# Kernel tuning notes

Measured on AMD Instinct MI355X. Metric: run time of the kernel, lower is better.

The kernel has to match this reference:

```python
import jax, jax.numpy as jnp
import numpy as np

NEG_SLOPE = 0.01  # nn.LeakyReLU default
N_NODES = 38332
POI_LEN = 38333
CAT_LEN = 400
POI_DIM = 300
CAT_DIM = 100
GCN_CH = 64
GCN_LAYERS = 5
N_EDGES = N_NODES * 32


def leaky(x):
    return jnp.where(x >= 0, x, NEG_SLOPE * x)


def gcn_conv(x, src, dst, W, b):
    """PyG GCNConv: add self loops + symmetric normalization.
    out = D^-1/2 (A+I) D^-1/2 X W + b, deg computed with self loops."""
    n = x.shape[0]
    h = x @ W  # [N, out]
    deg = jax.ops.segment_sum(jnp.ones_like(dst, dtype=h.dtype), dst, num_segments=n) + 1.0
    dinv = jax.lax.rsqrt(deg)  # deg >= 1 always (self loop)
    norm = dinv[src] * dinv[dst]  # [E]
    agg = jax.ops.segment_sum(h[src] * norm[:, None], dst, num_segments=n)
    agg = agg + h * (1.0 / deg)[:, None]  # self-loop term: norm_ii = 1/deg_i
    return agg + b


def setup_inputs() -> dict:
    key = jax.random.key(0)
    ks = jax.random.split(key, 16)
    poi_ids = jax.random.randint(ks[0], (N_NODES, 1), 0, POI_LEN).astype(jnp.float32)
    cat_ids = jax.random.randint(ks[1], (N_NODES, 1), 0, CAT_LEN).astype(jnp.float32)
    feats = jax.random.normal(ks[2], (N_NODES, 3), dtype=jnp.float32)
    x = jnp.concatenate([poi_ids, cat_ids, feats], axis=1)  # [N,5]
    edge_index = jax.random.randint(ks[3], (2, N_EDGES), 0, N_NODES, dtype=jnp.int32)

    def glorot(k, shape):
        lim = float(np.sqrt(6.0 / (shape[0] + shape[1])))
        return jax.random.uniform(k, shape, jnp.float32, -lim, lim)

    d_in = POI_DIM + CAT_DIM + 3  # 403
    params = {
        "poi_emb": jax.random.normal(ks[4], (POI_LEN, POI_DIM), jnp.float32),
        "cat_emb": jax.random.normal(ks[5], (CAT_LEN, CAT_DIM), jnp.float32),
        "W_in": glorot(ks[6], (d_in, GCN_CH)),
        "b_in": jnp.zeros((GCN_CH,), jnp.float32),
        "gcn_Ws": jnp.stack([glorot(jax.random.fold_in(ks[7], i), (GCN_CH, GCN_CH)) for i in range(GCN_LAYERS)]),
        "gcn_bs": jnp.zeros((GCN_LAYERS, GCN_CH), jnp.float32),
        "W_out": glorot(ks[8], (GCN_CH, 1)),
        "b_out": jnp.zeros((1,), jnp.float32),
        "fc1_W": glorot(ks[9], (N_NODES, 128)),
        "fc1_b": jnp.zeros((128,), jnp.float32),
        "fc2_W": glorot(ks[10], (128, POI_LEN)),
        "fc2_b": jnpos if False else jnp.zeros((POI_LEN,), jnp.float32),
    }
    return {"x": x, "edge_index": edge_index, **params}


def reference(x, edge_index, poi_emb, cat_emb, W_in, b_in, gcn_Ws, gcn_bs, W_out, b_out, fc1_W, fc1_b, fc2_W, fc2_b):
    src, dst = edge_index[0], edge_index[1]
    poi_f = poi_emb[x[:, 0].astype(jnp.int32)]  # [N,300]
    cat_f = cat_emb[x[:, 1].astype(jnp.int32)]  # [N,100]
    feat = jnp.concatenate([poi_f, cat_f, x[:, 2:5]], axis=1)  # [N,403]
    feat = leaky(gcn_conv(feat, src, dst, W_in, b_in))
    for i in range(GCN_LAYERS):
        t = gcn_conv(feat, src, dst, gcn_Ws[i], gcn_bs[i])
        feat = leaky(t) + t  # GcnUnit: relu(temp) + temp
    feat = leaky(gcn_conv(feat, src, dst, W_out, b_out)).reshape(-1)  # [N]
    h = jax.nn.relu(feat @ fc1_W + fc1_b)
    out = jax.nn.relu(h @ fc2_W + fc2_b)  # [poi_len]
    return out
```

## Files before the change

### kernel.cpp

```cpp
#include <hip/hip_runtime.h>
#include <hip/hip_bf16.h>

#define N_NODES 38332
#define POI_LEN 38333
#define CAT_LEN 400
#define POI_DIM 300
#define CAT_DIM 100
#define N_EDGES (N_NODES * 32)
#define NEG_SLOPE 0.01f
#define B1 ((N_NODES + 127) / 128)
#define SPLIT_CHUNK 4096
#define NSPLIT ((N_EDGES + SPLIT_CHUNK - 1) / SPLIT_CHUNK)
#define PLACE_CAP 8192
#define BCAP 8192

typedef __attribute__((ext_vector_type(8))) short short8;
typedef __attribute__((ext_vector_type(4))) float f32x4;

__device__ __forceinline__ unsigned short f2bf(float f) {
  unsigned u = __float_as_uint(f);
  u += 0x7fff + ((u >> 16) & 1);
  return (unsigned short)(u >> 16);
}
__device__ __forceinline__ float bflo(unsigned u) {
  return __uint_as_float(u << 16);
}
__device__ __forceinline__ float bfhi(unsigned u) {
  return __uint_as_float(u & 0xffff0000u);
}


#define WFIN_ELEMS (13 * 2048)
#define WFGCN_ELEMS (5 * 4096)

__global__ __launch_bounds__(256) void k_prep(const float* __restrict__ W_in,
                                              const float* __restrict__ gcn_Ws,
                                              unsigned short* __restrict__ wf_in,
                                              unsigned short* __restrict__ wf_gcn,
                                              int* __restrict__ bcnt,
                                              float* __restrict__ h128) {
  int idx = blockIdx.x * 256 + threadIdx.x;
  if (idx < B1) bcnt[idx] = 0;
  if (idx < 128) h128[idx] = 0.f;
  if (idx < WFIN_ELEMS) {
    int j = idx & 7, n = (idx >> 3) & 63, q = (idx >> 9) & 3, ks = idx >> 11;
    int k = ks * 32 + q * 8 + j;
    wf_in[idx] = f2bf((k < 400) ? W_in[k * 64 + n] : 0.f);
  } else if (idx < WFIN_ELEMS + WFGCN_ELEMS) {
    int t = idx - WFIN_ELEMS;
    int l = t >> 12, i = t & 4095;
    int j = i & 7, n = (i >> 3) & 63, q = (i >> 9) & 3, ks = i >> 11;
    int k = ks * 32 + q * 8 + j;
    wf_gcn[t] = f2bf(gcn_Ws[(size_t)l * 4096 + k * 64 + n]);
  }
}


__global__ __launch_bounds__(256) void k_split(const int* __restrict__ src,
                                               const int* __restrict__ dst,
                                               int* __restrict__ bcnt,
                                               int* __restrict__ staging) {
  __shared__ int hist[B1];
  __shared__ int lbase[B1];
  __shared__ int lcur[B1];
  int tid = threadIdx.x;
  int base = blockIdx.x * SPLIT_CHUNK;
  int n = N_EDGES - base;
  if (n > SPLIT_CHUNK) n = SPLIT_CHUNK;
  for (int b = tid; b < B1; b += 256) {
    hist[b] = 0;
    lcur[b] = 0;
  }
  __syncthreads();
  for (int i = tid; i < n; i += 256) atomicAdd(&hist[dst[base + i] >> 7], 1);
  __syncthreads();
  for (int b = tid; b < B1; b += 256) {
    int c = hist[b];
    lbase[b] = c ? atomicAdd(&bcnt[b], c) : 0;
  }
  __syncthreads();
  for (int i = tid; i < n; i += 256) {
    int d = dst[base + i];
    int s = src[base + i];
    int b = d >> 7;
    int off = atomicAdd(&lcur[b], 1);
    staging[(size_t)b * BCAP + lbase[b] + off] = (s << 7) | (d & 127);
  }
}

__global__ __launch_bounds__(256) void k_place(const int* __restrict__ staging,
                                               const int* __restrict__ bcnt,
                                               int* __restrict__ csr_src,
                                               int2* __restrict__ rs,
                                               float* __restrict__ dinv) {
  __shared__ int lc[128];
  __shared__ int ls[256];
  __shared__ int cur[128];
  __shared__ int buf[PLACE_CAP];
  int b = blockIdx.x;
  int tid = threadIdx.x;
  int d0 = b * 128;
  int nd = N_NODES - d0;
  if (nd > 128) nd = 128;
  int cnt_b = bcnt[b];
  const int* st = staging + (size_t)b * BCAP;
  if (tid < 128) lc[tid] = 0;
  __syncthreads();
  for (int i = tid; i < cnt_b; i += 256) atomicAdd(&lc[st[i] & 127], 1);
  __syncthreads();
  int v = (tid < 128) ? lc[tid] : 0;
  ls[tid] = v;
  __syncthreads();
  for (int off = 1; off < 128; off <<= 1) {
    int t = (tid >= off) ? ls[tid - off] : 0;
    __syncthreads();
    ls[tid] += t;
    __syncthreads();
  }
  if (tid < 128) {
    int excl = ls[tid] - v;
    cur[tid] = excl;
    if (tid < nd) {
      rs[d0 + tid] = make_int2(b * BCAP + excl, v);
      dinv[d0 + tid] = 1.0f / sqrtf((float)(v + 1));
    }
  }
  __syncthreads();
  for (int i = tid; i < cnt_b; i += 256) {
    int p = st[i];
    int pos = atomicAdd(&cur[p & 127], 1);
    buf[pos] = p >> 7;
  }
  __syncthreads();
  int base = b * BCAP;
  for (int i = tid; i < cnt_b; i += 256) csr_src[base + i] = buf[i];
}


__global__ __launch_bounds__(256) void k_front(
    const float* __restrict__ x, const float* __restrict__ poi_emb,
    const float* __restrict__ cat_emb, const float* __restrict__ W_in,
    const unsigned short* __restrict__ wf_in, const float* __restrict__ dinv,
    unsigned short* __restrict__ hs) {
  constexpr int KP = 416, RS = 424, NK4 = 104;
  __shared__ unsigned short sA[16 * RS];
  __shared__ float sC[16 * 68];
  __shared__ int sPid[16], sCid[16];
  __shared__ float sX[16][3];
  int tid = threadIdx.x;
  int row0 = blockIdx.x * 16;
  if (tid < 16) {
    int row = row0 + tid;
    if (row < N_NODES) {
      sPid[tid] = (int)x[row * 5 + 0];
      sCid[tid] = (int)x[row * 5 + 1];
      sX[tid][0] = x[row * 5 + 2];
      sX[tid][1] = x[row * 5 + 3];
      sX[tid][2] = x[row * 5 + 4];
    } else {
      sPid[tid] = 0; sCid[tid] = 0;
      sX[tid][0] = sX[tid][1] = sX[tid][2] = 0.f;
    }
  }
  __syncthreads();
  for (int idx = tid; idx < 16 * NK4; idx += 256) {
    int r = idx / NK4;
    int k = (idx - r * NK4) * 4;
    ushort4 o = {0, 0, 0, 0};
    if (k < 400 && row0 + r < N_NODES) {
      float4 f;
      if (k < 300) f = *(const float4*)(poi_emb + (size_t)sPid[r] * 300 + k);
      else         f = *(const float4*)(cat_emb + (size_t)sCid[r] * 100 + (k - 300));
      o.x = f2bf(f.x); o.y = f2bf(f.y); o.z = f2bf(f.z); o.w = f2bf(f.w);
    }
    *(ushort4*)&sA[r * RS + k] = o;
  }
  __syncthreads();
  int lane = tid & 63, wv = tid >> 6;
  int c = lane & 15, q = lane >> 4, n0 = wv * 16;
  f32x4 acc = {0.f, 0.f, 0.f, 0.f};
  const unsigned short* arow = &sA[c * RS];
#pragma unroll
  for (int ks = 0; ks < KP / 32; ks++) {
    short8 af = *(const short8*)(arow + ks * 32 + q * 8);
    short8 bf = *(const short8*)(wf_in + ((size_t)((ks * 4 + q) * 64 + n0 + c)) * 8);
    acc = __builtin_amdgcn_mfma_f32_16x16x32_bf16(af, bf, acc, 0, 0, 0);
  }
#pragma unroll
  for (int r = 0; r < 4; r++) sC[(q * 4 + r) * 68 + n0 + c] = acc[r];
  __syncthreads();
  for (int idx = tid; idx < 16 * 64; idx += 256) {
    int r = idx >> 6, col = idx & 63;
    int row = row0 + r;
    if (row < N_NODES) {
      float v = sC[r * 68 + col] + sX[r][0] * W_in[400 * 64 + col] +
                sX[r][1] * W_in[401 * 64 + col] + sX[r][2] * W_in[402 * 64 + col];
      hs[(size_t)row * 64 + col] = f2bf(v * dinv[row]);
    }
  }
}


__global__ __launch_bounds__(256) void k_projg(const unsigned short* __restrict__ A,
                                               const unsigned short* __restrict__ Wf,
                                               unsigned short* __restrict__ hs,
                                               const float* __restrict__ dinv) {
  constexpr int RS = 72;
  __shared__ unsigned short sA[16 * RS];
  __shared__ float sC[16 * 68];
  int tid = threadIdx.x;
  int row0 = blockIdx.x * 16;
  {
    int r = tid >> 4, k4 = (tid & 15) * 4;
    int row = row0 + r;
    ushort4 o = {0, 0, 0, 0};
    if (row < N_NODES) o = *(const ushort4*)(A + (size_t)row * 64 + k4);
    *(ushort4*)&sA[r * RS + k4] = o;
  }
  __syncthreads();
  int lane = tid & 63, wv = tid >> 6;
  int c = lane & 15, q = lane >> 4, n0 = wv * 16;
  f32x4 acc = {0.f, 0.f, 0.f, 0.f};
  const unsigned short* arow = &sA[c * RS];
#pragma unroll
  for (int ks = 0; ks < 2; ks++) {
    short8 af = *(const short8*)(arow + ks * 32 + q * 8);
    short8 bf = *(const short8*)(Wf + ((size_t)((ks * 4 + q) * 64 + n0 + c)) * 8);
    acc = __builtin_amdgcn_mfma_f32_16x16x32_bf16(af, bf, acc, 0, 0, 0);
  }
#pragma unroll
  for (int r = 0; r < 4; r++) sC[(q * 4 + r) * 68 + n0 + c] = acc[r];
  __syncthreads();
  for (int idx = tid; idx < 16 * 64; idx += 256) {
    int r = idx >> 6, col = idx & 63;
    int row = row0 + r;
    if (row < N_NODES) hs[(size_t)row * 64 + col] = f2bf(sC[r * 68 + col] * dinv[row]);
  }
}


template <int MODE>
__global__ __launch_bounds__(256) void k_agg(const unsigned short* __restrict__ hs,
                                             const int2* __restrict__ rs,
                                             const int* __restrict__ csr_src,
                                             const float* __restrict__ dinv,
                                             const float* __restrict__ bias,
                                             unsigned short* __restrict__ feat,
                                             const float* __restrict__ W_out,
                                             float* __restrict__ hs1) {
  int tid = threadIdx.x;
  int lane = tid & 63;
  int wv = tid >> 6;
  int node = blockIdx.x * 4 + wv;
  int eslot = lane >> 3;
  int ch8 = lane & 7;
  int2 rr = rs[node];
  int r0 = rr.x, r1 = rr.x + rr.y;
  float4 a0 = {0.f, 0.f, 0.f, 0.f}, a1 = a0;
#define ACC8(v)                                                              \
  do {                                                                       \
    a0.x += bflo((v).x); a0.y += bfhi((v).x);                                \
    a0.z += bflo((v).y); a0.w += bfhi((v).y);                                \
    a1.x += bflo((v).z); a1.y += bfhi((v).z);                                \
    a1.z += bflo((v).w); a1.w += bfhi((v).w);                                \
  } while (0)
  int e = r0 + eslot;
  for (; e + 24 < r1; e += 32) {
    int s0 = csr_src[e];
    int s1 = csr_src[e + 8];
    int s2 = csr_src[e + 16];
    int s3 = csr_src[e + 24];
    uint4 v0 = *(const uint4*)(hs + (size_t)s0 * 64 + ch8 * 8);
    uint4 v1 = *(const uint4*)(hs + (size_t)s1 * 64 + ch8 * 8);
    uint4 v2 = *(const uint4*)(hs + (size_t)s2 * 64 + ch8 * 8);
    uint4 v3 = *(const uint4*)(hs + (size_t)s3 * 64 + ch8 * 8);
    ACC8(v0); ACC8(v1); ACC8(v2); ACC8(v3);
  }
  if (e + 8 < r1) {
    int s0 = csr_src[e];
    int s1 = csr_src[e + 8];
    uint4 v0 = *(const uint4*)(hs + (size_t)s0 * 64 + ch8 * 8);
    uint4 v1 = *(const uint4*)(hs + (size_t)s1 * 64 + ch8 * 8);
    ACC8(v0); ACC8(v1);
    e += 16;
  }
  if (e < r1) {
    int s = csr_src[e];
    uint4 v = *(const uint4*)(hs + (size_t)s * 64 + ch8 * 8);
    ACC8(v);
  }
#undef ACC8
#pragma unroll
  for (int off = 8; off <= 32; off <<= 1) {
    a0.x += __shfl_xor(a0.x, off, 64);
    a0.y += __shfl_xor(a0.y, off, 64);
    a0.z += __shfl_xor(a0.z, off, 64);
    a0.w += __shfl_xor(a0.w, off, 64);
    a1.x += __shfl_xor(a1.x, off, 64);
    a1.y += __shfl_xor(a1.y, off, 64);
    a1.z += __shfl_xor(a1.z, off, 64);
    a1.w += __shfl_xor(a1.w, off, 64);
  }
  if (lane < 8) {
    uint4 sv = *(const uint4*)(hs + (size_t)node * 64 + ch8 * 8);
    float4 bb0 = *(const float4*)(bias + ch8 * 8);
    float4 bb1 = *(const float4*)(bias + ch8 * 8 + 4);
    float dn = dinv[node];
    float4 t0, t1;
    t0.x = dn * (a0.x + bflo(sv.x)) + bb0.x;
    t0.y = dn * (a0.y + bfhi(sv.x)) + bb0.y;
    t0.z = dn * (a0.z + bflo(sv.y)) + bb0.z;
    t0.w = dn * (a0.w + bfhi(sv.y)) + bb0.w;
    t1.x = dn * (a1.x + bflo(sv.z)) + bb1.x;
    t1.y = dn * (a1.y + bfhi(sv.z)) + bb1.y;
    t1.z = dn * (a1.z + bflo(sv.w)) + bb1.z;
    t1.w = dn * (a1.w + bfhi(sv.w)) + bb1.w;
    float4 l0, l1, o0, o1;
    l0.x = (t0.x >= 0.f) ? t0.x : NEG_SLOPE * t0.x;
    l0.y = (t0.y >= 0.f) ? t0.y : NEG_SLOPE * t0.y;
    l0.z = (t0.z >= 0.f) ? t0.z : NEG_SLOPE * t0.z;
    l0.w = (t0.w >= 0.f) ? t0.w : NEG_SLOPE * t0.w;
    l1.x = (t1.x >= 0.f) ? t1.x : NEG_SLOPE * t1.x;
    l1.y = (t1.y >= 0.f) ? t1.y : NEG_SLOPE * t1.y;
    l1.z = (t1.z >= 0.f) ? t1.z : NEG_SLOPE * t1.z;
    l1.w = (t1.w >= 0.f) ? t1.w : NEG_SLOPE * t1.w;
    if (MODE == 0) {
      o0 = l0; o1 = l1;
    } else {
      o0.x = l0.x + t0.x; o0.y = l0.y + t0.y; o0.z = l0.z + t0.z; o0.w = l0.w + t0.w;
      o1.x = l1.x + t1.x; o1.y = l1.y + t1.y; o1.z = l1.z + t1.z; o1.w = l1.w + t1.w;
    }
    if (MODE == 2) {
      float4 w0 = *(const float4*)(W_out + ch8 * 8);
      float4 w1 = *(const float4*)(W_out + ch8 * 8 + 4);
      float p = o0.x * w0.x + o0.y * w0.y + o0.z * w0.z + o0.w * w0.w +
                o1.x * w1.x + o1.y * w1.y + o1.z * w1.z + o1.w * w1.w;
      p += __shfl_xor(p, 1, 64);
      p += __shfl_xor(p, 2, 64);
      p += __shfl_xor(p, 4, 64);
      if (lane == 0) hs1[node] = p * dn;
    } else {
      uint4 pk;
      pk.x = (unsigned)f2bf(o0.x) | ((unsigned)f2bf(o0.y) << 16);
      pk.y = (unsigned)f2bf(o0.z) | ((unsigned)f2bf(o0.w) << 16);
      pk.z = (unsigned)f2bf(o1.x) | ((unsigned)f2bf(o1.y) << 16);
      pk.w = (unsigned)f2bf(o1.z) | ((unsigned)f2bf(o1.w) << 16);
      *(uint4*)(feat + (size_t)node * 64 + ch8 * 8) = pk;
    }
  }
}


__global__ __launch_bounds__(256) void k_out_agg(const float* __restrict__ hs1,
                                                 const int2* __restrict__ rs,
                                                 const int* __restrict__ csr_src,
                                                 const float* __restrict__ dinv,
                                                 const float* __restrict__ b_out,
                                                 float* __restrict__ g) {
  int lane = threadIdx.x & 63;
  int w = threadIdx.x >> 6;
  int node = blockIdx.x * 4 + w;
  int2 rr = rs[node];
  int r0 = rr.x, r1 = rr.x + rr.y;
  float acc = 0.f;
  for (int e = r0 + lane; e < r1; e += 64) acc += hs1[csr_src[e]];
#pragma unroll
  for (int off = 32; off; off >>= 1) acc += __shfl_xor(acc, off, 64);
  if (lane == 0) {
    float t = dinv[node] * (acc + hs1[node]) + b_out[0];
    g[node] = (t >= 0.f) ? t : NEG_SLOPE * t;
  }
}


__global__ __launch_bounds__(128) void k_fc1(const float* __restrict__ g,
                                             const float* __restrict__ fc1_W,
                                             float* __restrict__ h128) {
  int j = threadIdx.x;
  int base = blockIdx.x * 32;
  int end = base + 32;
  if (end > N_NODES) end = N_NODES;
  float acc = 0.f;
  int i = base;
  for (; i + 4 <= end; i += 4) {
    acc += g[i + 0] * fc1_W[(size_t)(i + 0) * 128 + j];
    acc += g[i + 1] * fc1_W[(size_t)(i + 1) * 128 + j];
    acc += g[i + 2] * fc1_W[(size_t)(i + 2) * 128 + j];
    acc += g[i + 3] * fc1_W[(size_t)(i + 3) * 128 + j];
  }
  for (; i < end; i++) acc += g[i] * fc1_W[(size_t)i * 128 + j];
  atomicAdd(&h128[j], acc);
}

__global__ __launch_bounds__(256) void k_fc2(const float* __restrict__ h128raw,
                                             const float* __restrict__ fc1_b,
                                             const float* __restrict__ fc2_W,
                                             const float* __restrict__ fc2_b,
                                             float* __restrict__ out) {
  __shared__ float sh[128];
  int tid = threadIdx.x;
  if (tid < 128) {
    float v = h128raw[tid] + fc1_b[tid];
    sh[tid] = (v > 0.f) ? v : 0.f;
  }
  __syncthreads();
  int p = blockIdx.x * 256 + tid;
  if (p < POI_LEN) {
    float acc = fc2_b[p];
#pragma unroll 8
    for (int j = 0; j < 128; j++) acc += sh[j] * fc2_W[(size_t)j * POI_LEN + p];
    out[p] = (acc > 0.f) ? acc : 0.f;
  }
}


extern "C" void kernel_launch(void* const* d_in, const int* in_sizes, int n_in,
                              void* d_out, int out_size, void* d_ws, size_t ws_size,
                              hipStream_t stream) {
  const float* x       = (const float*)d_in[0];
  const int*   ei      = (const int*)d_in[1];
  const float* poi_emb = (const float*)d_in[2];
  const float* cat_emb = (const float*)d_in[3];
  const float* W_in    = (const float*)d_in[4];
  const float* b_in    = (const float*)d_in[5];
  const float* gcn_Ws  = (const float*)d_in[6];
  const float* gcn_bs  = (const float*)d_in[7];
  const float* W_out   = (const float*)d_in[8];
  const float* b_out   = (const float*)d_in[9];
  const float* fc1_W   = (const float*)d_in[10];
  const float* fc1_b   = (const float*)d_in[11];
  const float* fc2_W   = (const float*)d_in[12];
  const float* fc2_b   = (const float*)d_in[13];
  const int* src = ei;
  const int* dst = ei + N_EDGES;

  char* p = (char*)d_ws;
  auto take = [&](size_t bytes) {
    char* r = p;
    p += (bytes + 255) & ~(size_t)255;
    return r;
  };
  int2*  rs        = (int2*)take((size_t)N_NODES * 8);
  float* dinv      = (float*)take((size_t)N_NODES * 4);
  int*   bcnt      = (int*)take((size_t)B1 * 4);
  int*   csr_src   = (int*)take((size_t)B1 * BCAP * 4);
  unsigned short* feat = (unsigned short*)take((size_t)N_NODES * 64 * 2);
  unsigned short* hs   = (unsigned short*)take((size_t)N_NODES * 64 * 2);
  float* hs1       = (float*)take((size_t)N_NODES * 4);
  float* g         = (float*)take((size_t)N_NODES * 4);
  float* h128      = (float*)take(128 * 4);
  unsigned short* wf_in  = (unsigned short*)take((size_t)WFIN_ELEMS * 2);
  unsigned short* wf_gcn = (unsigned short*)take((size_t)WFGCN_ELEMS * 2);
  int* staging = (int*)feat;
  float* out = (float*)d_out;

  const int nb4 = N_NODES / 4;
  const int nb16 = (N_NODES + 15) / 16;

  k_prep<<<(WFIN_ELEMS + WFGCN_ELEMS + 255) / 256, 256, 0, stream>>>(
      W_in, gcn_Ws, wf_in, wf_gcn, bcnt, h128);
  k_split<<<NSPLIT, 256, 0, stream>>>(src, dst, bcnt, staging);
  k_place<<<B1, 256, 0, stream>>>(staging, bcnt, csr_src, rs, dinv);

  k_front<<<nb16, 256, 0, stream>>>(x, poi_emb, cat_emb, W_in, wf_in, dinv, hs);

  k_agg<0><<<nb4, 256, 0, stream>>>(hs, rs, csr_src, dinv, b_in, feat, nullptr,
                                    nullptr);
  for (int l = 0; l < 5; l++) {
    k_projg<<<nb16, 256, 0, stream>>>(feat, wf_gcn + (size_t)l * 4096, hs, dinv);
    if (l < 4)
      k_agg<1><<<nb4, 256, 0, stream>>>(hs, rs, csr_src, dinv,
                                        gcn_bs + (size_t)l * 64, feat, nullptr,
                                        nullptr);
    else
      k_agg<2><<<nb4, 256, 0, stream>>>(hs, rs, csr_src, dinv,
                                        gcn_bs + (size_t)l * 64, nullptr, W_out,
                                        hs1);
  }

  k_out_agg<<<nb4, 256, 0, stream>>>(hs1, rs, csr_src, dinv, b_out, g);
  k_fc1<<<(N_NODES + 31) / 32, 128, 0, stream>>>(g, fc1_W, h128);
  k_fc2<<<(POI_LEN + 255) / 256, 256, 0, stream>>>(h128, fc1_b, fc2_W, fc2_b, out);
}
```

Baseline: 433.9 us.

## Fuse next-layer projection into aggregation kernel and halve split chunk size

The separate k_projg kernel is removed. Each aggregation block now writes its four activated node rows into shared memory and runs the next layer's 64x64 bf16 MFMA projection in place, writing hs for the next layer directly. Ping-pong buffers replace the feat/hs pair. This drops five kernel launches and the round trip of the intermediate feature array through global memory. The cost is one MFMA tile that wastes 12 of its 16 rows (zero padded), plus extra syncs in a gather-bound kernel. SPLIT_CHUNK is also halved to get more blocks in the edge split pass.

```diff
diff --git a/kernel.cpp b/kernel.cpp
--- a/kernel.cpp
+++ b/kernel.cpp
@@ -9,7 +9,7 @@
 #define N_EDGES (N_NODES * 32)
 #define NEG_SLOPE 0.01f
 #define B1 ((N_NODES + 127) / 128)
-#define SPLIT_CHUNK 4096
+#define SPLIT_CHUNK 2048
 #define NSPLIT ((N_EDGES + SPLIT_CHUNK - 1) / SPLIT_CHUNK)
 #define PLACE_CAP 8192
 #define BCAP 8192
@@ -201,59 +201,28 @@
 }
 
 
-__global__ __launch_bounds__(256) void k_projg(const unsigned short* __restrict__ A,
-                                               const unsigned short* __restrict__ Wf,
-                                               unsigned short* __restrict__ hs,
-                                               const float* __restrict__ dinv) {
-  constexpr int RS = 72;
-  __shared__ unsigned short sA[16 * RS];
-  __shared__ float sC[16 * 68];
-  int tid = threadIdx.x;
-  int row0 = blockIdx.x * 16;
-  {
-    int r = tid >> 4, k4 = (tid & 15) * 4;
-    int row = row0 + r;
-    ushort4 o = {0, 0, 0, 0};
-    if (row < N_NODES) o = *(const ushort4*)(A + (size_t)row * 64 + k4);
-    *(ushort4*)&sA[r * RS + k4] = o;
-  }
-  __syncthreads();
-  int lane = tid & 63, wv = tid >> 6;
-  int c = lane & 15, q = lane >> 4, n0 = wv * 16;
-  f32x4 acc = {0.f, 0.f, 0.f, 0.f};
-  const unsigned short* arow = &sA[c * RS];
-#pragma unroll
-  for (int ks = 0; ks < 2; ks++) {
-    short8 af = *(const short8*)(arow + ks * 32 + q * 8);
-    short8 bf = *(const short8*)(Wf + ((size_t)((ks * 4 + q) * 64 + n0 + c)) * 8);
-    acc = __builtin_amdgcn_mfma_f32_16x16x32_bf16(af, bf, acc, 0, 0, 0);
-  }
-#pragma unroll
-  for (int r = 0; r < 4; r++) sC[(q * 4 + r) * 68 + n0 + c] = acc[r];
-  __syncthreads();
-  for (int idx = tid; idx < 16 * 64; idx += 256) {
-    int r = idx >> 6, col = idx & 63;
-    int row = row0 + r;
-    if (row < N_NODES) hs[(size_t)row * 64 + col] = f2bf(sC[r * 68 + col] * dinv[row]);
-  }
-}
-
-
 template <int MODE>
 __global__ __launch_bounds__(256) void k_agg(const unsigned short* __restrict__ hs,
                                              const int2* __restrict__ rs,
                                              const int* __restrict__ csr_src,
                                              const float* __restrict__ dinv,
                                              const float* __restrict__ bias,
-                                             unsigned short* __restrict__ feat,
+                                             const unsigned short* __restrict__ Wf,
+                                             unsigned short* __restrict__ hs_next,
                                              const float* __restrict__ W_out,
                                              float* __restrict__ hs1) {
+  __shared__ unsigned short sA[16 * 72];
+  __shared__ float sC[4 * 68];
   int tid = threadIdx.x;
   int lane = tid & 63;
   int wv = tid >> 6;
   int node = blockIdx.x * 4 + wv;
   int eslot = lane >> 3;
   int ch8 = lane & 7;
+  if (MODE != 2) {
+    for (int i = tid; i < 216; i += 256)
+      *(ushort4*)&sA[288 + i * 4] = (ushort4){0, 0, 0, 0};
+  }
   int2 rr = rs[node];
   int r0 = rr.x, r1 = rr.x + rr.y;
   float4 a0 = {0.f, 0.f, 0.f, 0.f}, a1 = a0;
@@ -301,11 +270,11 @@
     a1.z += __shfl_xor(a1.z, off, 64);
     a1.w += __shfl_xor(a1.w, off, 64);
   }
+  float dn = dinv[node];
   if (lane < 8) {
     uint4 sv = *(const uint4*)(hs + (size_t)node * 64 + ch8 * 8);
     float4 bb0 = *(const float4*)(bias + ch8 * 8);
     float4 bb1 = *(const float4*)(bias + ch8 * 8 + 4);
-    float dn = dinv[node];
     float4 t0, t1;
     t0.x = dn * (a0.x + bflo(sv.x)) + bb0.x;
     t0.y = dn * (a0.y + bfhi(sv.x)) + bb0.y;
@@ -345,7 +314,32 @@
       pk.y = (unsigned)f2bf(o0.z) | ((unsigned)f2bf(o0.w) << 16);
       pk.z = (unsigned)f2bf(o1.x) | ((unsigned)f2bf(o1.y) << 16);
       pk.w = (unsigned)f2bf(o1.z) | ((unsigned)f2bf(o1.w) << 16);
-      *(uint4*)(feat + (size_t)node * 64 + ch8 * 8) = pk;
+      *(uint4*)&sA[wv * 72 + ch8 * 8] = pk;
+    }
+  }
+  if (MODE != 2) {
+    __syncthreads();
+    int c = lane & 15, q = lane >> 4, n0 = wv * 16;
+    f32x4 acc = {0.f, 0.f, 0.f, 0.f};
+    const unsigned short* arow = &sA[c * 72];
+#pragma unroll
+    for (int ks = 0; ks < 2; ks++) {
+      short8 af = *(const short8*)(arow + ks * 32 + q * 8);
+      short8 bf = *(const short8*)(Wf + ((size_t)((ks * 4 + q) * 64 + n0 + c)) * 8);
+      acc = __builtin_amdgcn_mfma_f32_16x16x32_bf16(af, bf, acc, 0, 0, 0);
+    }
+    if (q == 0) {
+#pragma unroll
+      for (int r = 0; r < 4; r++) sC[r * 68 + n0 + c] = acc[r];
+    }
+    __syncthreads();
+    if (tid < 128) {
+      int r = tid >> 5, c2 = (tid & 31) * 2;
+      int row = blockIdx.x * 4 + r;
+      float dr = dinv[row];
+      unsigned lo = f2bf(sC[r * 68 + c2] * dr);
+      unsigned hi = f2bf(sC[r * 68 + c2 + 1] * dr);
+      *(unsigned*)(hs_next + (size_t)row * 64 + c2) = lo | (hi << 16);
     }
   }
 }
@@ -444,14 +438,14 @@
   float* dinv      = (float*)take((size_t)N_NODES * 4);
   int*   bcnt      = (int*)take((size_t)B1 * 4);
   int*   csr_src   = (int*)take((size_t)B1 * BCAP * 4);
-  unsigned short* feat = (unsigned short*)take((size_t)N_NODES * 64 * 2);
-  unsigned short* hs   = (unsigned short*)take((size_t)N_NODES * 64 * 2);
+  unsigned short* hsA = (unsigned short*)take((size_t)N_NODES * 64 * 2);
+  unsigned short* hsB = (unsigned short*)take((size_t)N_NODES * 64 * 2);
   float* hs1       = (float*)take((size_t)N_NODES * 4);
   float* g         = (float*)take((size_t)N_NODES * 4);
   float* h128      = (float*)take(128 * 4);
   unsigned short* wf_in  = (unsigned short*)take((size_t)WFIN_ELEMS * 2);
   unsigned short* wf_gcn = (unsigned short*)take((size_t)WFGCN_ELEMS * 2);
-  int* staging = (int*)feat;
+  int* staging = (int*)hsA;
   float* out = (float*)d_out;
 
   const int nb4 = N_NODES / 4;
@@ -462,21 +456,20 @@
   k_split<<<NSPLIT, 256, 0, stream>>>(src, dst, bcnt, staging);
   k_place<<<B1, 256, 0, stream>>>(staging, bcnt, csr_src, rs, dinv);
 
-  k_front<<<nb16, 256, 0, stream>>>(x, poi_emb, cat_emb, W_in, wf_in, dinv, hs);
-
-  k_agg<0><<<nb4, 256, 0, stream>>>(hs, rs, csr_src, dinv, b_in, feat, nullptr,
-                                    nullptr);
-  for (int l = 0; l < 5; l++) {
-    k_projg<<<nb16, 256, 0, stream>>>(feat, wf_gcn + (size_t)l * 4096, hs, dinv);
-    if (l < 4)
-      k_agg<1><<<nb4, 256, 0, stream>>>(hs, rs, csr_src, dinv,
-                                        gcn_bs + (size_t)l * 64, feat, nullptr,
-                                        nullptr);
-    else
-      k_agg<2><<<nb4, 256, 0, stream>>>(hs, rs, csr_src, dinv,
-                                        gcn_bs + (size_t)l * 64, nullptr, W_out,
-                                        hs1);
-  }
+  k_front<<<nb16, 256, 0, stream>>>(x, poi_emb, cat_emb, W_in, wf_in, dinv, hsA);
+
+  k_agg<0><<<nb4, 256, 0, stream>>>(hsA, rs, csr_src, dinv, b_in,
+                                    wf_gcn + 0 * 4096, hsB, nullptr, nullptr);
+  k_agg<1><<<nb4, 256, 0, stream>>>(hsB, rs, csr_src, dinv, gcn_bs + 0 * 64,
+                                    wf_gcn + 1 * 4096, hsA, nullptr, nullptr);
+  k_agg<1><<<nb4, 256, 0, stream>>>(hsA, rs, csr_src, dinv, gcn_bs + 1 * 64,
+                                    wf_gcn + 2 * 4096, hsB, nullptr, nullptr);
+  k_agg<1><<<nb4, 256, 0, stream>>>(hsB, rs, csr_src, dinv, gcn_bs + 2 * 64,
+                                    wf_gcn + 3 * 4096, hsA, nullptr, nullptr);
+  k_agg<1><<<nb4, 256, 0, stream>>>(hsA, rs, csr_src, dinv, gcn_bs + 3 * 64,
+                                    wf_gcn + 4 * 4096, hsB, nullptr, nullptr);
+  k_agg<2><<<nb4, 256, 0, stream>>>(hsB, rs, csr_src, dinv, gcn_bs + 4 * 64,
+                                    nullptr, nullptr, W_out, hs1);
 
   k_out_agg<<<nb4, 256, 0, stream>>>(hs1, rs, csr_src, dinv, b_out, g);
   k_fc1<<<(N_NODES + 31) / 32, 128, 0, stream>>>(g, fc1_W, h128);
```

New measurement: 408.2 us (median of 2 runs). 5.9% less time.
